# Kernel tuning notes

Hardware: AMD Instinct MI355X
Metric: run time of the kernel (lower is better)

Reference implementation:

```python
import jax, jax.numpy as jnp
import numpy as np

# Uniform-scope sizes: B molecules, A atoms/mol, G fragments/mol, W map width,
# H hidden, L attention layers, S = G+1 (fg prompt row prepended per molecule)
B, A, G, W, H, L = 1024, 64, 31, 8, 512, 2
S = G + 1
DK = 32  # attention head dim (hard-coded in the module)


def _layernorm(x, g, b, eps):
    mu = jnp.mean(x, axis=-1, keepdims=True)
    var = jnp.var(x, axis=-1, keepdims=True)
    return g * (x - mu) * jax.lax.rsqrt(var + eps) + b


def setup_inputs() -> dict:
    key = jax.random.key(0)
    ks = jax.random.split(key, 16)
    s = 0.02
    return {
        "f_atom": jax.random.normal(ks[0], (B * A, H), jnp.float32),
        "f_group": jax.random.normal(ks[1], (B * G, H), jnp.float32),
        "fg": jax.random.normal(ks[2], (1, 3 * H), jnp.float32),
        "alpha": 0.1 * jnp.ones((1,), jnp.float32),
        "lr_w": jax.random.normal(ks[3], (3 * H, H), jnp.float32) * s,
        "lr_b": jnp.zeros((H,), jnp.float32),
        "wq_w": jax.random.normal(ks[4], (L, H, DK), jnp.float32) * s,
        "wq_b": jnp.zeros((L, DK), jnp.float32),
        "wk_w": jax.random.normal(ks[5], (L, H, DK), jnp.float32) * s,
        "wk_b": jnp.zeros((L, DK), jnp.float32),
        "wv_w": jax.random.normal(ks[6], (L, H, DK), jnp.float32) * s,
        "wv_b": jnp.zeros((L, DK), jnp.float32),
        "dense_w": jax.random.normal(ks[7], (L, DK, H), jnp.float32) * s,
        "dense_b": jnp.zeros((L, H), jnp.float32),
        "ln_g": jnp.ones((L, H), jnp.float32),
        "ln_b": jnp.zeros((L, H), jnp.float32),
        "lin_w": jax.random.normal(ks[8], (H, H), jnp.float32) * s,
        "lin_b": jnp.zeros((H,), jnp.float32),
        "norm_g": jnp.ones((H,), jnp.float32),
        "norm_b": jnp.zeros((H,), jnp.float32),
        "mapping": jax.random.randint(ks[9], (B * G, W), 0, A + 1, jnp.int64),
    }


def reference(f_atom, f_group, fg, alpha, lr_w, lr_b, wq_w, wq_b, wk_w, wk_b,
              wv_w, wv_b, dense_w, dense_b, ln_g, ln_b, lin_w, lin_b,
              norm_g, norm_b, mapping):
    # --- ragged gather + reduce + pad (vectorized: uniform scopes) ---
    a = f_atom.reshape(B, A, H)
    # prepend zero padding row per molecule (mapping index 0 -> zeros)
    a_pad = jnp.concatenate([jnp.zeros((B, 1, H), a.dtype), a], axis=1)  # [B,A+1,H]
    m = mapping.reshape(B, G, W)
    gathered = a_pad[jnp.arange(B)[:, None, None], m]  # [B,G,W,H]
    g = f_group.reshape(B, G, H)
    cur_g = jnp.concatenate(
        [gathered.sum(axis=2), gathered.max(axis=2), g], axis=-1)  # [B,G,3H]
    brics = jnp.concatenate(
        [jnp.broadcast_to(fg[None], (B, 1, 3 * H)), cur_g], axis=1)  # [B,S,3H]

    f_frag = jax.nn.relu(brics @ lr_w + lr_b)  # [B,S,H]

    # mask built from init_hiddens = f_frag (same for every layer)
    pm = (f_frag != 0).astype(f_frag.dtype)
    mask = jnp.einsum('bsh,bth->bst', pm, pm)  # [B,S,S]
    neg = jnp.asarray(-1e9, f_frag.dtype)
    scale = 1.0 / np.sqrt(DK)

    hs = f_frag
    attn = None
    for l in range(L):
        q = hs @ wq_w[l] + wq_b[l]
        k = hs @ wk_w[l] + wk_b[l]
        v = hs @ wv_w[l] + wv_b[l]
        scores = jnp.einsum('bsd,btd->bst', q, k) * scale
        scores = jnp.where(mask == 0, neg, scores)
        attn = jax.nn.softmax(scores, axis=-1)
        x = jnp.einsum('bst,btd->bsd', attn, v)
        dh = x @ dense_w[l] + dense_b[l]  # dropout is identity in eval
        hs = _layernorm(dh + hs, ln_g[l], ln_b[l], 1e-6)

    f_out = _layernorm(hs @ lin_w + lin_b, norm_g, norm_b, 1e-5) * alpha[0]
    return f_out[:, 0, :], attn
```

## Files before the change

kernel.cpp:

```cpp
#include <hip/hip_runtime.h>

#define B_   1024
#define A_   64
#define G_   31
#define W_   8
#define H_   512
#define L_   2
#define S_   32
#define DK_  32
#define K3H_ 1536

typedef short short8 __attribute__((ext_vector_type(8)));
typedef float floatx4 __attribute__((ext_vector_type(4)));

__device__ __forceinline__ float bf2f(unsigned short u){
  union { unsigned int i; float f; } x; x.i = ((unsigned int)u) << 16; return x.f;
}
__device__ __forceinline__ unsigned short f2bf(float f){
  union { float f; unsigned int i; } x; x.f = f;
  unsigned int u = x.i;
  return (unsigned short)((u + 0x7FFFu + ((u >> 16) & 1u)) >> 16);
}
__device__ __forceinline__ unsigned int pack2bf(float a, float b){
  return (unsigned int)f2bf(a) | ((unsigned int)f2bf(b) << 16);
}
__device__ __forceinline__ void gl_lds16(const unsigned short* g, unsigned short* l){
  __builtin_amdgcn_global_load_lds((const __attribute__((address_space(1))) unsigned int*)g,
                                   (__attribute__((address_space(3))) unsigned int*)l, 16, 0, 0);
}

__global__ __launch_bounds__(512) void prep_and_build(
    const float* __restrict__ f_atom, const float* __restrict__ f_group,
    const float* __restrict__ fg, const int* __restrict__ mapping,
    const float* __restrict__ lr_w, const float* __restrict__ lin_w,
    const float* __restrict__ wq_w, const float* __restrict__ wk_w, const float* __restrict__ wv_w,
    const float* __restrict__ dense_w,
    unsigned short* __restrict__ brics,
    unsigned short* __restrict__ lr_wT, unsigned short* __restrict__ lin_wT,
    unsigned short* __restrict__ qkvT, unsigned short* __restrict__ denseT){
  __shared__ __align__(16) float ldsf[8192];
  int bx = blockIdx.x;
  int tid = threadIdx.x;

  if (bx < 4096){
    int b = bx >> 2, qc = bx & 3;
    int kb = qc * 128;
    int wave = tid >> 6, lane = tid & 63;
    const float* fa = f_atom + (size_t)b * A_ * H_ + kb;
    #pragma unroll
    for (int j = 0; j < 4; ++j){
      int f = j*512 + tid;
      int r = f >> 5, c4v = f & 31;
      *(float4*)&ldsf[r*128 + c4v*4] = *(const float4*)(fa + (size_t)r*H_ + c4v*4);
    }
    __syncthreads();
    int c2 = lane * 2;
    #pragma unroll
    for (int q = 0; q < 4; ++q){
      int s = wave*4 + q;
      if (s == 0) continue;
      int g = s - 1;
      unsigned short* out = brics + (size_t)(b*32 + s) * K3H_ + kb;
      const int* mp = mapping + ((size_t)(b * G_ + g)) * W_;
      int4 m0 = *(const int4*)mp;
      int4 m1 = *(const int4*)(mp + 4);
      int id[8] = {m0.x, m0.y, m0.z, m0.w, m1.x, m1.y, m1.z, m1.w};
      float sum0 = 0.f, sum1 = 0.f;
      float mx0 = -3.4e38f, mx1 = -3.4e38f;
      #pragma unroll
      for (int w = 0; w < 8; ++w){
        int r = id[w] > 0 ? id[w] - 1 : 0;
        float2 v = *(const float2*)&ldsf[r*128 + c2];
        bool z = (id[w] == 0);
        float v0 = z ? 0.f : v.x, v1 = z ? 0.f : v.y;
        sum0 += v0; sum1 += v1;
        mx0 = fmaxf(mx0, v0); mx1 = fmaxf(mx1, v1);
      }
      *(unsigned int*)(out + c2)       = pack2bf(sum0, sum1);
      *(unsigned int*)(out + 512 + c2) = pack2bf(mx0, mx1);
    }
    return;
  }

  if (bx < 8064){
    int pair = (bx - 4096) * 8 + (tid >> 6);
    int c0 = (tid & 63) * 8;
    int b = pair / G_, g = pair - b * G_;
    const float* src = f_group + (size_t)pair * H_ + c0;
    float4 v0 = *(const float4*)src;
    float4 v1 = *(const float4*)(src + 4);
    unsigned short o[8] __attribute__((aligned(16)));
    o[0]=f2bf(v0.x); o[1]=f2bf(v0.y); o[2]=f2bf(v0.z); o[3]=f2bf(v0.w);
    o[4]=f2bf(v1.x); o[5]=f2bf(v1.y); o[6]=f2bf(v1.z); o[7]=f2bf(v1.w);
    *(uint4*)(brics + (size_t)(b*32 + g + 1) * K3H_ + 1024 + c0) = *(const uint4*)o;
    return;
  }

  if (bx < 8448){
    int e = (bx - 8064) * 4096 + tid * 8;
    int batch = e / K3H_, c = e - batch * K3H_;
    const float* src = fg + c;
    float4 v0 = *(const float4*)src;
    float4 v1 = *(const float4*)(src + 4);
    unsigned short o[8] __attribute__((aligned(16)));
    o[0]=f2bf(v0.x); o[1]=f2bf(v0.y); o[2]=f2bf(v0.z); o[3]=f2bf(v0.w);
    o[4]=f2bf(v1.x); o[5]=f2bf(v1.y); o[6]=f2bf(v1.z); o[7]=f2bf(v1.w);
    *(uint4*)(brics + (size_t)batch*32*K3H_ + c) = *(const uint4*)o;
    return;
  }

  if (bx < 8704){
    int tb = bx - 8448;
    const float* src; unsigned short* dst; int R, C;
    if (tb < 192){ src = lr_w;  dst = lr_wT;  R = 1536; C = 512; }
    else         { tb -= 192; src = lin_w; dst = lin_wT; R = 512;  C = 512; }
    int rt = tb >> 3, ct = tb & 7;
    if (tid < 256){
      int r16 = tid >> 4, c4 = tid & 15;
      #pragma unroll
      for (int p = 0; p < 4; ++p){
        int row = p*16 + r16;
        float4 v = *(const float4*)(src + (size_t)(rt*64 + row) * C + ct*64 + c4*4);
        ldsf[row*65 + c4*4+0] = v.x; ldsf[row*65 + c4*4+1] = v.y;
        ldsf[row*65 + c4*4+2] = v.z; ldsf[row*65 + c4*4+3] = v.w;
      }
    }
    __syncthreads();
    if (tid < 256){
      int rr = tid >> 3, cc8 = tid & 7;
      #pragma unroll
      for (int p = 0; p < 2; ++p){
        int n = p*32 + rr;
        unsigned short o[8] __attribute__((aligned(16)));
        #pragma unroll
        for (int j = 0; j < 8; ++j) o[j] = f2bf(ldsf[(cc8*8 + j)*65 + n]);
        *(uint4*)(dst + (size_t)(ct*64 + n) * R + rt*64 + cc8*8) = *(const uint4*)o;
      }
    }
    return;
  }

  int i = (bx - 8704) * 512 + tid;
  if (i < 98304){
    int k = i & 511; int t = i >> 9; int n = t & 31; int u = t >> 5;
    int p = u % 3, l = u / 3;
    const float* src = (p == 0) ? wq_w : (p == 1) ? wk_w : wv_w;
    qkvT[((size_t)((l*3+p)*S_ + n)) * H_ + k] = f2bf(src[((size_t)(l*H_ + k)) * DK_ + n]);
    return;
  }
  i -= 98304;
  if (i < 32768){
    int k = i & 31; int t = i >> 5; int n = t & 511; int l = t >> 9;
    denseT[((size_t)(l*H_ + n)) * DK_ + k] = f2bf(dense_w[((size_t)(l*DK_ + k)) * H_ + n]);
  }
}

__global__ __launch_bounds__(256) void gemm_frag(
    const unsigned short* __restrict__ brics, const unsigned short* __restrict__ wT,
    const float* __restrict__ lr_b, unsigned short* __restrict__ f_frag){
  __shared__ __align__(16) unsigned short As[128*64];
  __shared__ __align__(16) unsigned short Bs[128*64];
  int tid = threadIdx.x;
  int bx = blockIdx.x;
  int xcd = bx & 7, slot = bx >> 3;
  int mtile = xcd + 8 * (slot >> 2);
  int ntile = slot & 3;
  int rowStart = mtile * 128, colStart = ntile * 128;
  int lane = tid & 63, wave = tid >> 6;
  int m16 = lane & 15, quad = lane >> 4;
  int wm = wave >> 1, wn = wave & 1;
  floatx4 acc[4][4];
  #pragma unroll
  for (int i = 0; i < 4; ++i)
    #pragma unroll
    for (int j = 0; j < 4; ++j) acc[i][j] = (floatx4){0.f,0.f,0.f,0.f};

  int srow = tid >> 3;
  int gchunk = (tid & 7) ^ (srow & 7);
  size_t aOff[4], bOff[4];
  #pragma unroll
  for (int p = 0; p < 4; ++p){
    aOff[p] = (size_t)(rowStart + p*32 + srow) * K3H_ + gchunk*8;
    bOff[p] = (size_t)(colStart + p*32 + srow) * K3H_ + gchunk*8;
  }
  int fsw0 = ((0*4 + quad) ^ (m16 & 7)) * 8;
  int fsw1 = ((1*4 + quad) ^ (m16 & 7)) * 8;

  for (int kt = 0; kt < K3H_/64; ++kt){
    int kbase = kt * 64;
    #pragma unroll
    for (int p = 0; p < 4; ++p){
      gl_lds16(brics + aOff[p] + kbase, As + p*2048 + (size_t)tid*8);
      gl_lds16(wT    + bOff[p] + kbase, Bs + p*2048 + (size_t)tid*8);
    }
    __syncthreads();
    #pragma unroll
    for (int ks = 0; ks < 2; ++ks){
      int fsw = ks ? fsw1 : fsw0;
      short8 af[4], bfr[4];
      #pragma unroll
      for (int i = 0; i < 4; ++i){
        af[i]  = *(const short8*)(As + (wm*64 + i*16 + m16)*64 + fsw);
        bfr[i] = *(const short8*)(Bs + (wn*64 + i*16 + m16)*64 + fsw);
      }
      #pragma unroll
      for (int i = 0; i < 4; ++i)
        #pragma unroll
        for (int j = 0; j < 4; ++j)
          acc[i][j] = __builtin_amdgcn_mfma_f32_16x16x32_bf16(af[i], bfr[j], acc[i][j], 0, 0, 0);
    }
    __syncthreads();
  }
  #pragma unroll
  for (int i = 0; i < 4; ++i)
    #pragma unroll
    for (int j = 0; j < 4; ++j){
      int col = colStart + wn*64 + j*16 + m16;
      float bias = lr_b[col];
      #pragma unroll
      for (int r = 0; r < 4; ++r){
        int row = rowStart + wm*64 + i*16 + quad*4 + r;
        float v = acc[i][j][r] + bias;
        v = v > 0.f ? v : 0.f;
        f_frag[(size_t)row * H_ + col] = f2bf(v);
      }
    }
}

__global__ __launch_bounds__(256) void attn_kernel(
    const unsigned short* __restrict__ f_frag,
    const unsigned short* __restrict__ qkvT, const unsigned short* __restrict__ denseT,
    const float* __restrict__ wq_b, const float* __restrict__ wk_b, const float* __restrict__ wv_b,
    const float* __restrict__ dense_b, const float* __restrict__ ln_g, const float* __restrict__ ln_b,
    unsigned short* __restrict__ hsf, float* __restrict__ out_attn){
  const int HP = 552, TP = 40;
  __shared__ __align__(16) unsigned short hs[S_*552];
  __shared__ __align__(16) unsigned short Qs[S_*40];
  __shared__ __align__(16) unsigned short Ks[S_*40];
  __shared__ __align__(16) unsigned short Vt[S_*40];
  __shared__ __align__(16) unsigned short Ps[S_*40];
  __shared__ __align__(16) unsigned short Xs[S_*40];
  __shared__ unsigned long long pmask[S_*8];
  __shared__ unsigned int mz[S_];
  int b = blockIdx.x;
  int tid = threadIdx.x;
  int wave = tid >> 6, lane = tid & 63;
  int m16 = lane & 15, quad = lane >> 4;

  {
    int row = tid >> 3, cc = (tid & 7) * 64;
    const unsigned short* src = f_frag + ((size_t)(b * S_ + row)) * H_ + cc;
    unsigned short* dst = hs + row * HP + cc;
    #pragma unroll
    for (int k = 0; k < 64; k += 8)
      *(uint4*)(dst + k) = *(const uint4*)(src + k);
  }
  if (tid < S_) mz[tid] = 0u;
  __syncthreads();
  {
    int s = tid >> 3, w = tid & 7;
    const unsigned short* hrow = hs + s * HP + w * 64;
    unsigned long long m = 0ull;
    #pragma unroll
    for (int c = 0; c < 64; c += 8){
      short8 hv = *(const short8*)(hrow + c);
      #pragma unroll
      for (int j = 0; j < 8; ++j)
        if ((unsigned short)hv[j] != 0) m |= (1ull << (c + j));
    }
    pmask[s * 8 + w] = m;
  }
  __syncthreads();
  for (int idx = tid; idx < S_*S_; idx += 256){
    int s = idx >> 5, t2 = idx & 31;
    bool inter = false;
    #pragma unroll
    for (int w = 0; w < 8; ++w)
      inter = inter || ((pmask[s*8+w] & pmask[t2*8+w]) != 0ull);
    if (!inter) atomicOr(&mz[s], 1u << t2);
  }
  __syncthreads();

  const float scale = 0.17677669529663687f;
  for (int l = 0; l < L_; ++l){
    {
      int mt = wave >> 1, nt = wave & 1;
      floatx4 aq = {0,0,0,0}, ak = {0,0,0,0}, av = {0,0,0,0};
      const unsigned short* arow = hs + (mt*16 + m16) * HP + quad*8;
      const unsigned short* bq = qkvT + ((size_t)((l*3 + 0)*S_ + nt*16 + m16)) * H_ + quad*8;
      const unsigned short* bk = bq + (size_t)S_ * H_;
      const unsigned short* bv = bk + (size_t)S_ * H_;
      for (int k0 = 0; k0 < H_; k0 += 32){
        short8 a = *(const short8*)(arow + k0);
        aq = __builtin_amdgcn_mfma_f32_16x16x32_bf16(a, *(const short8*)(bq + k0), aq, 0,0,0);
        ak = __builtin_amdgcn_mfma_f32_16x16x32_bf16(a, *(const short8*)(bk + k0), ak, 0,0,0);
        av = __builtin_amdgcn_mfma_f32_16x16x32_bf16(a, *(const short8*)(bv + k0), av, 0,0,0);
      }
      int col = nt*16 + m16;
      float bqs = wq_b[l*DK_ + col], bks = wk_b[l*DK_ + col], bvs = wv_b[l*DK_ + col];
      #pragma unroll
      for (int r = 0; r < 4; ++r){
        int rw = mt*16 + quad*4 + r;
        Qs[rw*TP + col] = f2bf((aq[r] + bqs) * scale);
        Ks[rw*TP + col] = f2bf(ak[r] + bks);
        Vt[col*TP + rw] = f2bf(av[r] + bvs);
      }
    }
    __syncthreads();
    if (wave < 2){
      int mt = wave;
      short8 a  = *(const short8*)(Qs + (mt*16 + m16)*TP + quad*8);
      short8 b0 = *(const short8*)(Ks + m16*TP + quad*8);
      short8 b1 = *(const short8*)(Ks + (16 + m16)*TP + quad*8);
      floatx4 z = {0,0,0,0};
      floatx4 s0 = __builtin_amdgcn_mfma_f32_16x16x32_bf16(a, b0, z, 0,0,0);
      floatx4 s1 = __builtin_amdgcn_mfma_f32_16x16x32_bf16(a, b1, z, 0,0,0);
      #pragma unroll
      for (int r = 0; r < 4; ++r){
        int s = mt*16 + quad*4 + r;
        unsigned int m = mz[s];
        float v0 = ((m >> m16) & 1u) ? -1e9f : s0[r];
        float v1 = ((m >> (16 + m16)) & 1u) ? -1e9f : s1[r];
        float mx = fmaxf(v0, v1);
        #pragma unroll
        for (int d = 1; d < 16; d <<= 1) mx = fmaxf(mx, __shfl_xor(mx, d));
        float e0 = __expf(v0 - mx), e1 = __expf(v1 - mx);
        float sm = e0 + e1;
        #pragma unroll
        for (int d = 1; d < 16; d <<= 1) sm += __shfl_xor(sm, d);
        float inv = 1.f / sm;
        float p0 = e0 * inv, p1 = e1 * inv;
        Ps[s*TP + m16] = f2bf(p0);
        Ps[s*TP + 16 + m16] = f2bf(p1);
        if (l == L_ - 1){
          float* oa = out_attn + ((size_t)b * S_ + s) * S_;
          oa[m16] = p0; oa[16 + m16] = p1;
        }
      }
    }
    __syncthreads();
    {
      int mt = wave >> 1, nt = wave & 1;
      short8 a  = *(const short8*)(Ps + (mt*16 + m16)*TP + quad*8);
      short8 bv = *(const short8*)(Vt + (nt*16 + m16)*TP + quad*8);
      floatx4 z = {0,0,0,0};
      floatx4 x = __builtin_amdgcn_mfma_f32_16x16x32_bf16(a, bv, z, 0,0,0);
      #pragma unroll
      for (int r = 0; r < 4; ++r)
        Xs[(mt*16 + quad*4 + r)*TP + nt*16 + m16] = f2bf(x[r]);
    }
    __syncthreads();
    {
      short8 bx0 = *(const short8*)(Xs + m16*TP + quad*8);
      short8 bx1 = *(const short8*)(Xs + (16 + m16)*TP + quad*8);
      #pragma unroll
      for (int j = 0; j < 8; ++j){
        int dct = wave*8 + j;
        short8 aw = *(const short8*)(denseT + ((size_t)(l*H_ + dct*16 + m16)) * DK_ + quad*8);
        floatx4 z = {0,0,0,0};
        floatx4 d0 = __builtin_amdgcn_mfma_f32_16x16x32_bf16(aw, bx0, z, 0,0,0);
        floatx4 d1 = __builtin_amdgcn_mfma_f32_16x16x32_bf16(aw, bx1, z, 0,0,0);
        int dc0 = dct*16 + quad*4;
        float4 db4 = *(const float4*)(dense_b + l*H_ + dc0);
        const float dbr[4] = {db4.x, db4.y, db4.z, db4.w};
        unsigned short* h0 = hs + m16*HP + dc0;
        unsigned short* h1 = hs + (16 + m16)*HP + dc0;
        unsigned long long u0 = *(unsigned long long*)h0;
        unsigned long long u1 = *(unsigned long long*)h1;
        unsigned long long o0 = 0ull, o1 = 0ull;
        #pragma unroll
        for (int r = 0; r < 4; ++r){
          float hv0 = bf2f((unsigned short)(u0 >> (16*r)));
          float hv1 = bf2f((unsigned short)(u1 >> (16*r)));
          o0 |= (unsigned long long)f2bf(d0[r] + dbr[r] + hv0) << (16*r);
          o1 |= (unsigned long long)f2bf(d1[r] + dbr[r] + hv1) << (16*r);
        }
        *(unsigned long long*)h0 = o0;
        *(unsigned long long*)h1 = o1;
      }
    }
    __syncthreads();
    {
      #pragma unroll
      for (int rr = 0; rr < 8; ++rr){
        int row = wave*8 + rr;
        unsigned short* hrow = hs + row*HP + lane*8;
        short8 hv = *(const short8*)hrow;
        float v[8]; float s1 = 0.f, s2 = 0.f;
        #pragma unroll
        for (int j = 0; j < 8; ++j){ v[j] = bf2f((unsigned short)hv[j]); s1 += v[j]; s2 += v[j]*v[j]; }
        #pragma unroll
        for (int d = 1; d < 64; d <<= 1){ s1 += __shfl_xor(s1, d); s2 += __shfl_xor(s2, d); }
        float mean = s1 * (1.f/512.f);
        float var = s2 * (1.f/512.f) - mean*mean;
        float rs = rsqrtf(var + 1e-6f);
        unsigned short o[8] __attribute__((aligned(16)));
        #pragma unroll
        for (int j = 0; j < 8; ++j){
          int colj = lane*8 + j;
          float nv = (v[j] - mean) * rs * ln_g[l*H_ + colj] + ln_b[l*H_ + colj];
          o[j] = f2bf(nv);
        }
        *(uint4*)hrow = *(const uint4*)o;
      }
    }
    __syncthreads();
  }
  if (tid < 64){
    *(uint4*)(hsf + (size_t)b * H_ + tid*8) = *(const uint4*)(hs + tid*8);
  }
}

__global__ __launch_bounds__(256) void final_kernel(
    const unsigned short* __restrict__ hsf, const unsigned short* __restrict__ lin_wT,
    const float* __restrict__ lin_b, const float* __restrict__ norm_g, const float* __restrict__ norm_b,
    const float* __restrict__ alpha, float* __restrict__ out_f){
  const int HP = 552;
  __shared__ __align__(16) unsigned short hsb[32*552];
  int blk = blockIdx.x;
  int tid = threadIdx.x;
  int wave = tid >> 6, lane = tid & 63;
  int m16 = lane & 15, quad = lane >> 4;
  {
    int row = tid >> 3, cc = (tid & 7) * 64;
    const unsigned short* src = hsf + ((size_t)(blk*32 + row)) * H_ + cc;
    unsigned short* dst = hsb + row*HP + cc;
    #pragma unroll
    for (int k = 0; k < 64; k += 8)
      *(uint4*)(dst + k) = *(const uint4*)(src + k);
  }
  __syncthreads();
  floatx4 acc[2][8];
  #pragma unroll
  for (int mt = 0; mt < 2; ++mt)
    #pragma unroll
    for (int j = 0; j < 8; ++j) acc[mt][j] = (floatx4){0.f,0.f,0.f,0.f};
  for (int k0 = 0; k0 < H_; k0 += 32){
    short8 a0 = *(const short8*)(hsb + m16*HP + k0 + quad*8);
    short8 a1 = *(const short8*)(hsb + (16 + m16)*HP + k0 + quad*8);
    #pragma unroll
    for (int j = 0; j < 8; ++j){
      int n = (wave*8 + j)*16 + m16;
      short8 bw = *(const short8*)(lin_wT + (size_t)n * H_ + k0 + quad*8);
      acc[0][j] = __builtin_amdgcn_mfma_f32_16x16x32_bf16(a0, bw, acc[0][j], 0,0,0);
      acc[1][j] = __builtin_amdgcn_mfma_f32_16x16x32_bf16(a1, bw, acc[1][j], 0,0,0);
    }
  }
  __syncthreads();
  #pragma unroll
  for (int mt = 0; mt < 2; ++mt)
    #pragma unroll
    for (int j = 0; j < 8; ++j){
      int col = (wave*8 + j)*16 + m16;
      float lb = lin_b[col];
      #pragma unroll
      for (int r = 0; r < 4; ++r){
        int row = mt*16 + quad*4 + r;
        hsb[row*HP + col] = f2bf(acc[mt][j][r] + lb);
      }
    }
  __syncthreads();
  float al = alpha[0];
  #pragma unroll
  for (int rr = 0; rr < 8; ++rr){
    int row = wave*8 + rr;
    const unsigned short* hrow = hsb + row*HP + lane*8;
    short8 hv = *(const short8*)hrow;
    float v[8]; float s1 = 0.f, s2 = 0.f;
    #pragma unroll
    for (int j = 0; j < 8; ++j){ v[j] = bf2f((unsigned short)hv[j]); s1 += v[j]; s2 += v[j]*v[j]; }
    #pragma unroll
    for (int d = 1; d < 64; d <<= 1){ s1 += __shfl_xor(s1, d); s2 += __shfl_xor(s2, d); }
    float mean = s1 * (1.f/512.f);
    float var = s2 * (1.f/512.f) - mean*mean;
    float rs = rsqrtf(var + 1e-5f);
    float o[8];
    #pragma unroll
    for (int j = 0; j < 8; ++j){
      int colj = lane*8 + j;
      o[j] = ((v[j] - mean) * rs * norm_g[colj] + norm_b[colj]) * al;
    }
    float* op = out_f + ((size_t)(blk*32 + row)) * H_ + lane*8;
    float4 f0 = {o[0], o[1], o[2], o[3]};
    float4 f1 = {o[4], o[5], o[6], o[7]};
    *(float4*)op = f0;
    *(float4*)(op + 4) = f1;
  }
}

extern "C" void kernel_launch(void* const* d_in, const int* in_sizes, int n_in,
                              void* d_out, int out_size, void* d_ws, size_t ws_size,
                              hipStream_t stream){
  const float* f_atom  = (const float*)d_in[0];
  const float* f_group = (const float*)d_in[1];
  const float* fg      = (const float*)d_in[2];
  const float* alpha   = (const float*)d_in[3];
  const float* lr_w    = (const float*)d_in[4];
  const float* lr_b    = (const float*)d_in[5];
  const float* wq_w    = (const float*)d_in[6];
  const float* wq_b    = (const float*)d_in[7];
  const float* wk_w    = (const float*)d_in[8];
  const float* wk_b    = (const float*)d_in[9];
  const float* wv_w    = (const float*)d_in[10];
  const float* wv_b    = (const float*)d_in[11];
  const float* dense_w = (const float*)d_in[12];
  const float* dense_b = (const float*)d_in[13];
  const float* ln_g    = (const float*)d_in[14];
  const float* ln_b    = (const float*)d_in[15];
  const float* lin_w   = (const float*)d_in[16];
  const float* lin_b   = (const float*)d_in[17];
  const float* norm_g  = (const float*)d_in[18];
  const float* norm_b  = (const float*)d_in[19];
  const int*   mapping = (const int*)d_in[20];

  unsigned short* brics  = (unsigned short*)d_ws;
  unsigned short* f_frag = brics  + (size_t)32768 * 1536;
  unsigned short* lr_wT  = f_frag + (size_t)32768 * 512;
  unsigned short* qkvT   = lr_wT  + (size_t)512 * 1536;
  unsigned short* denseT = qkvT   + (size_t)2*3*32*512;
  unsigned short* lin_wT = denseT + (size_t)2*512*32;
  unsigned short* hsf    = lin_wT + (size_t)512*512;

  float* out_f    = (float*)d_out;
  float* out_attn = out_f + (size_t)B_ * H_;

  prep_and_build<<<8960, 512, 0, stream>>>(f_atom, f_group, fg, mapping,
                                           lr_w, lin_w, wq_w, wk_w, wv_w, dense_w,
                                           brics, lr_wT, lin_wT, qkvT, denseT);
  gemm_frag<<<(32768/128) * (512/128), 256, 0, stream>>>(brics, lr_wT, lr_b, f_frag);
  attn_kernel<<<B_, 256, 0, stream>>>(f_frag, qkvT, denseT, wq_b, wk_b, wv_b,
                                      dense_b, ln_g, ln_b, hsf, out_attn);
  final_kernel<<<B_/32, 256, 0, stream>>>(hsf, lin_wT, lin_b, norm_g, norm_b, alpha, out_f);
}
```

Baseline: 456.2 us.

## Interleave gather and streaming blocks; load atoms via global_load_lds with zero row

The prep kernel now interleaves atom-gather blocks with the other streaming-conversion blocks in the grid order, so the LDS-heavy and pure bandwidth blocks share the GPU concurrently. Atom tiles are loaded directly into LDS with global_load_lds instead of going through registers. An extra zero row is appended in LDS so padding indices read zeros, which removes the per-element select in the gather loop. LDS use per block grows slightly, and the changed grid mapping must still cover every block exactly.

New measurement: 465.6 us. +2.1%, slower.

```diff
diff --git a/kernel.cpp b/kernel.cpp
--- a/kernel.cpp
+++ b/kernel.cpp
@@ -28,6 +28,10 @@
   __builtin_amdgcn_global_load_lds((const __attribute__((address_space(1))) unsigned int*)g,
                                    (__attribute__((address_space(3))) unsigned int*)l, 16, 0, 0);
 }
+__device__ __forceinline__ void gl_lds16f(const float* g, float* l){
+  __builtin_amdgcn_global_load_lds((const __attribute__((address_space(1))) unsigned int*)g,
+                                   (__attribute__((address_space(3))) unsigned int*)l, 16, 0, 0);
+}
 
 __global__ __launch_bounds__(512) void prep_and_build(
     const float* __restrict__ f_atom, const float* __restrict__ f_group,
@@ -38,12 +42,16 @@
     unsigned short* __restrict__ brics,
     unsigned short* __restrict__ lr_wT, unsigned short* __restrict__ lin_wT,
     unsigned short* __restrict__ qkvT, unsigned short* __restrict__ denseT){
-  __shared__ __align__(16) float ldsf[8192];
+  __shared__ __align__(16) float ldsf[65*128];
   int bx = blockIdx.x;
   int tid = threadIdx.x;
 
-  if (bx < 4096){
-    int b = bx >> 2, qc = bx & 3;
+  bool isGather = (bx < 8192) && ((bx & 1) == 0);
+  int sid = (bx < 8192) ? (bx >> 1) : (4096 + (bx - 8192));
+
+  if (isGather){
+    int gb = bx >> 1;
+    int b = gb >> 2, qc = gb & 3;
     int kb = qc * 128;
     int wave = tid >> 6, lane = tid & 63;
     const float* fa = f_atom + (size_t)b * A_ * H_ + kb;
@@ -51,8 +59,9 @@
     for (int j = 0; j < 4; ++j){
       int f = j*512 + tid;
       int r = f >> 5, c4v = f & 31;
-      *(float4*)&ldsf[r*128 + c4v*4] = *(const float4*)(fa + (size_t)r*H_ + c4v*4);
-    }
+      gl_lds16f(fa + (size_t)r*H_ + c4v*4, &ldsf[f*4]);
+    }
+    if (tid < 32) *(float4*)&ldsf[64*128 + tid*4] = (float4){0.f,0.f,0.f,0.f};
     __syncthreads();
     int c2 = lane * 2;
     #pragma unroll
@@ -69,12 +78,10 @@
       float mx0 = -3.4e38f, mx1 = -3.4e38f;
       #pragma unroll
       for (int w = 0; w < 8; ++w){
-        int r = id[w] > 0 ? id[w] - 1 : 0;
+        int r = id[w] > 0 ? id[w] - 1 : 64;
         float2 v = *(const float2*)&ldsf[r*128 + c2];
-        bool z = (id[w] == 0);
-        float v0 = z ? 0.f : v.x, v1 = z ? 0.f : v.y;
-        sum0 += v0; sum1 += v1;
-        mx0 = fmaxf(mx0, v0); mx1 = fmaxf(mx1, v1);
+        sum0 += v.x; sum1 += v.y;
+        mx0 = fmaxf(mx0, v.x); mx1 = fmaxf(mx1, v.y);
       }
       *(unsigned int*)(out + c2)       = pack2bf(sum0, sum1);
       *(unsigned int*)(out + 512 + c2) = pack2bf(mx0, mx1);
@@ -82,8 +89,8 @@
     return;
   }
 
-  if (bx < 8064){
-    int pair = (bx - 4096) * 8 + (tid >> 6);
+  if (sid < 3968){
+    int pair = sid * 8 + (tid >> 6);
     int c0 = (tid & 63) * 8;
     int b = pair / G_, g = pair - b * G_;
     const float* src = f_group + (size_t)pair * H_ + c0;
@@ -96,8 +103,8 @@
     return;
   }
 
-  if (bx < 8448){
-    int e = (bx - 8064) * 4096 + tid * 8;
+  if (sid < 4352){
+    int e = (sid - 3968) * 4096 + tid * 8;
     int batch = e / K3H_, c = e - batch * K3H_;
     const float* src = fg + c;
     float4 v0 = *(const float4*)src;
@@ -109,8 +116,8 @@
     return;
   }
 
-  if (bx < 8704){
-    int tb = bx - 8448;
+  if (sid < 4608){
+    int tb = sid - 4352;
     const float* src; unsigned short* dst; int R, C;
     if (tb < 192){ src = lr_w;  dst = lr_wT;  R = 1536; C = 512; }
     else         { tb -= 192; src = lin_w; dst = lin_wT; R = 512;  C = 512; }
@@ -140,7 +147,7 @@
     return;
   }
 
-  int i = (bx - 8704) * 512 + tid;
+  int i = (sid - 4608) * 512 + tid;
   if (i < 98304){
     int k = i & 511; int t = i >> 9; int n = t & 31; int u = t >> 5;
     int p = u % 3, l = u / 3;
```
